# Kernel optimization log

Measured on AMD Instinct MI355X. Metric: run time of the kernel, lower is better.

## Reference

```python
import jax, jax.numpy as jnp
import numpy as np

EPS = 1e-5

def _layernorm(h, g, b):
    mu = jnp.mean(h, axis=-1, keepdims=True)
    var = jnp.mean((h - mu) ** 2, axis=-1, keepdims=True)
    return (h - mu) / jnp.sqrt(var + EPS) * g + b

def _linoss_scan_im(A, dt, Bu):
    # A, dt: (N,) real; Bu: (B, L, N) complex64.
    # IM discretization of z' = -A x + B u, x' = z (LinOSS paper Eq. 3-4),
    # computed with a 2x2 block-diagonal associative (parallel) scan.
    S = 1.0 / (1.0 + dt * dt * A)  # Schur complement
    m11 = 1.0 - dt * dt * A * S
    m12 = -dt * A * S
    m21 = dt * S
    m22 = S
    fz = (m11 * dt) * Bu
    fx = (m21 * dt) * Bu
    Bt, L, N = Bu.shape
    br = lambda m: jnp.broadcast_to(m.astype(Bu.dtype), (Bt, L, N))
    elems = (br(m11), br(m12), br(m21), br(m22), fz, fx)

    def binop(ei, ej):
        a11i, a12i, a21i, a22i, bzi, bxi = ei
        a11j, a12j, a21j, a22j, bzj, bxj = ej
        return (a11j * a11i + a12j * a21i,
                a11j * a12i + a12j * a22i,
                a21j * a11i + a22j * a21i,
                a21j * a12i + a22j * a22i,
                a11j * bzi + a12j * bxi + bzj,
                a21j * bzi + a22j * bxi + bxj)

    res = jax.lax.associative_scan(binop, elems, axis=1)
    return res[5]  # x-component of the state, (B, L, N) complex

def setup_inputs():
    key = jax.random.key(0)
    ks = jax.random.split(key, 20)
    B, L, H_in, D_mod = 8, 2048, 128, 512
    s_in = np.float32(1.0 / np.sqrt(H_in))
    s_d = np.float32(1.0 / np.sqrt(D_mod))
    f32 = jnp.float32
    return {
        "x": jax.random.normal(ks[0], (B, L, H_in), f32),
        "W_in": jax.random.normal(ks[1], (D_mod, H_in), f32) * s_in,
        "b_in": jnp.zeros((D_mod,), f32),
        "W_enc": jax.random.normal(ks[2], (D_mod, D_mod), f32) * s_d,
        "b_enc": jnp.zeros((D_mod,), f32),
        "ln_g": jnp.ones((D_mod,), f32),
        "ln_b": jnp.zeros((D_mod,), f32),
        "A_diag": jax.random.uniform(ks[3], (D_mod,), f32),
        "log_steps": jax.random.normal(ks[4], (D_mod,), f32) * 0.5,
        "B_re": jax.random.normal(ks[5], (D_mod, D_mod), f32) * s_d,
        "B_im": jax.random.normal(ks[6], (D_mod, D_mod), f32) * s_d,
        "C_re": jax.random.normal(ks[7], (D_mod, D_mod), f32) * s_d,
        "C_im": jax.random.normal(ks[8], (D_mod, D_mod), f32) * s_d,
        "D": jax.random.normal(ks[9], (D_mod,), f32),
        "glu_w1": jax.random.normal(ks[10], (D_mod, D_mod), f32) * s_d,
        "glu_b1": jnp.zeros((D_mod,), f32),
        "glu_w2": jax.random.normal(ks[11], (D_mod, D_mod), f32) * s_d,
        "glu_b2": jnp.zeros((D_mod,), f32),
        "W_dec": jax.random.normal(ks[12], (D_mod, D_mod), f32) * s_d,
        "b_dec": jnp.zeros((D_mod,), f32),
        "W_out": jax.random.normal(ks[13], (H_in, D_mod), f32) * s_d,
        "b_out": jnp.zeros((H_in,), f32),
    }

def reference(x, W_in, b_in, W_enc, b_enc, ln_g, ln_b, A_diag, log_steps,
              B_re, B_im, C_re, C_im, D, glu_w1, glu_b1, glu_w2, glu_b2,
              W_dec, b_dec, W_out, b_out):
    h = x @ W_in.T + b_in                       # outer in_proj: (B, L, d)
    h = h @ W_enc.T + b_enc                     # LinOSS encoder
    skip = h
    hn = _layernorm(h, ln_g, ln_b)
    A = jax.nn.relu(A_diag)                     # nonnegative oscillator freqs
    dt = jax.nn.sigmoid(log_steps)              # per-state timestep in (0,1)
    Bc = (B_re + 1j * B_im).astype(jnp.complex64)
    Cc = (C_re + 1j * C_im).astype(jnp.complex64)
    Bu = jnp.einsum('blh,nh->bln', hn.astype(jnp.complex64), Bc)
    xs = _linoss_scan_im(A, dt, Bu)             # (B, L, N) complex
    y = jnp.einsum('bln,hn->blh', xs, Cc).real + D * hn
    y = jax.nn.gelu(y)
    y = (y @ glu_w1.T + glu_b1) * jax.nn.sigmoid(y @ glu_w2.T + glu_b2)  # GLU
    h = skip + y                                # residual (dropout = eval mode)
    h = h @ W_dec.T + b_dec                     # LinOSS decoder
    return h @ W_out.T + b_out                  # outer out_proj: (B, L, out)
```

## Files before the change

### kernel.cpp

```cpp
#include <hip/hip_runtime.h>
#include <cstddef>
#include <cstdint>
#include <math.h>

typedef _Float16 f16;
typedef f16 f16x8 __attribute__((ext_vector_type(8)));
typedef f16 f16x4 __attribute__((ext_vector_type(4)));
typedef float f32x4 __attribute__((ext_vector_type(4)));

constexpr int Bb   = 8;
constexpr int Ll   = 2048;
constexpr int Hin  = 128;
constexpr int Dm   = 512;
constexpr int Mrows = Bb * Ll;
constexpr int NC   = 32;
constexpr int CL   = Ll / NC;
constexpr int SZ1  = Bb * NC * Dm;

constexpr int TILE_ELE = 128 * 64;

static __device__ __forceinline__ float sigmoid_f(float x) {
    return 1.f / (1.f + expf(-x));
}
static __device__ __forceinline__ float gelu_tanh_f(float x) {
    float x3 = x * x * x;
    float t  = tanhf(0.7978845608028654f * (x + 0.044715f * x3));
    return 0.5f * x * (1.f + t);
}

static __device__ __forceinline__ void gld16(const f16* g, f16* l) {
    __builtin_amdgcn_global_load_lds(
        (const __attribute__((address_space(1))) void*)g,
        (__attribute__((address_space(3))) void*)l, 16, 0, 0);
}

__global__ __launch_bounds__(128) void fuse_wc1(
    const float* __restrict__ Wenc, const float* __restrict__ Win,
    const float* __restrict__ b_in, const float* __restrict__ b_enc,
    f16* __restrict__ Wc1, float* __restrict__ bc1)
{
    const int d2 = blockIdx.x;
    const int t  = threadIdx.x;
    float acc = 0.f;
    for (int d = 0; d < Dm; ++d)
        acc = fmaf(Wenc[d2 * Dm + d], Win[d * Hin + t], acc);
    Wc1[d2 * Hin + t] = (f16)acc;
    if (t == 0) {
        float s = 0.f;
        for (int d = 0; d < Dm; ++d) s = fmaf(Wenc[d2 * Dm + d], b_in[d], s);
        bc1[d2] = s + b_enc[d2];
    }
}

__global__ __launch_bounds__(512) void fuse_wc2(
    const float* __restrict__ Wout, const float* __restrict__ Wdec,
    const float* __restrict__ b_dec, const float* __restrict__ b_out,
    f16* __restrict__ Wc2, float* __restrict__ bc2)
{
    const int o = blockIdx.x;
    const int t = threadIdx.x;
    float acc = 0.f;
    for (int d = 0; d < Dm; ++d)
        acc = fmaf(Wout[o * Dm + d], Wdec[d * Dm + t], acc);
    Wc2[o * Dm + t] = (f16)acc;
    if (t == 0) {
        float s = 0.f;
        for (int d = 0; d < Dm; ++d) s = fmaf(Wout[o * Dm + d], b_dec[d], s);
        bc2[o] = s + b_out[o];
    }
}

struct CvtJob { const float* s; f16* d; int n; };
struct CvtJobs { CvtJob j[7]; };

__global__ __launch_bounds__(256) void convert_k(CvtJobs jobs) {
    const CvtJob jb = jobs.j[blockIdx.y];
    const int i = (blockIdx.x * 256 + threadIdx.x) * 4;
    if (i >= jb.n) return;
    const float4 v = *(const float4*)(jb.s + i);
    f16x4 o;
    o.x = (f16)v.x; o.y = (f16)v.y; o.z = (f16)v.z; o.w = (f16)v.w;
    *(f16x4*)(jb.d + i) = o;
}

template <int KM, int OUTF16>
__global__ __launch_bounds__(256) void gemm_mfma(
    const f16* __restrict__ A, const f16* __restrict__ A2,
    const f16* __restrict__ W, const f16* __restrict__ W2,
    const float* __restrict__ bias,
    const f16* __restrict__ EX, const f16* __restrict__ EX2,
    const float* __restrict__ DV,
    void* __restrict__ Cout, int M, int N, int K)
{
    __shared__ f16 smem[4 * TILE_ELE];

    const int tid = threadIdx.x;
    const int l   = tid & 63;
    const int wid = tid >> 6;
    const int wr  = wid >> 1;
    const int wc  = wid & 1;
    const int lc  = l & 15;
    const int lr  = l >> 4;
    const int row0 = blockIdx.x * 128;
    const int col0 = blockIdx.y * 128;

    const int Kst = (KM == 1) ? Dm : K;
    const int KL  = (KM == 1) ? 2 * Dm : K;
    const int NT  = KL >> 6;

    const int swz  = (l & 7) << 4;
    const int off0 = ((lr * 16) ^ swz) >> 1;
    const int off1 = ((64 + lr * 16) ^ swz) >> 1;

    f32x4 acc[4][4];
#pragma unroll
    for (int i = 0; i < 4; ++i)
#pragma unroll
        for (int j = 0; j < 4; ++j) acc[i][j] = (f32x4){0.f, 0.f, 0.f, 0.f};

    auto asrc = [&](int k0) -> const f16* {
        if (KM == 1 && k0 >= Dm) return A2 + (size_t)row0 * Dm + (k0 - Dm);
        return A + (size_t)row0 * Kst + k0;
    };
    auto wsrc = [&](int k0) -> const f16* {
        if (KM == 1 && k0 >= Dm) return W2 + (size_t)col0 * Dm + (k0 - Dm);
        return W + (size_t)col0 * Kst + k0;
    };

#define STAGE(DST, SRC)                                                      \
    {                                                                        \
        _Pragma("unroll")                                                    \
        for (int c = 0; c < 4; ++c) {                                        \
            const int chunk = c * 256 + tid;                                 \
            const int row   = chunk >> 3;                                    \
            const int kb    = ((chunk & 7) << 4) ^ ((row & 7) << 4);         \
            gld16(SRC + (size_t)row * Kst + (kb >> 1), DST + chunk * 8);     \
        }                                                                    \
    }

    STAGE(smem, asrc(0));
    STAGE(smem + 2 * TILE_ELE, wsrc(0));
    __syncthreads();

    int cur = 0;
    for (int kt = 0; kt < NT; ++kt) {
        if (kt + 1 < NT) {
            STAGE(smem + (cur ^ 1) * TILE_ELE, asrc((kt + 1) << 6));
            STAGE(smem + (2 + (cur ^ 1)) * TILE_ELE, wsrc((kt + 1) << 6));
        }
        const f16* Asc = smem + cur * TILE_ELE;
        const f16* Bsc = smem + (2 + cur) * TILE_ELE;
#pragma unroll
        for (int ks = 0; ks < 2; ++ks) {
            const int off = ks ? off1 : off0;
            f16x8 aF[4], bF[4];
#pragma unroll
            for (int mi = 0; mi < 4; ++mi)
                aF[mi] = *(const f16x8*)(Asc + (wr * 64 + mi * 16 + lc) * 64 + off);
#pragma unroll
            for (int ni = 0; ni < 4; ++ni)
                bF[ni] = *(const f16x8*)(Bsc + (wc * 64 + ni * 16 + lc) * 64 + off);
#pragma unroll
            for (int mi = 0; mi < 4; ++mi)
#pragma unroll
                for (int ni = 0; ni < 4; ++ni)
                    acc[mi][ni] = __builtin_amdgcn_mfma_f32_16x16x32_f16(
                        aF[mi], bF[ni], acc[mi][ni], 0, 0, 0);
        }
        __syncthreads();
        cur ^= 1;
    }
#undef STAGE

    float* Cf32 = (float*)Cout;
    f16*   Cf16 = (f16*)Cout;
#pragma unroll
    for (int mi = 0; mi < 4; ++mi) {
#pragma unroll
        for (int ni = 0; ni < 4; ++ni) {
            const int col   = col0 + wc * 64 + ni * 16 + lc;
            const int rbase = row0 + wr * 64 + mi * 16 + lr * 4;
            const f32x4 v = acc[mi][ni];
            if (KM == 0) {
                const float bv = bias ? bias[col] : 0.f;
#pragma unroll
                for (int r = 0; r < 4; ++r) {
                    const float o = v[r] + bv;
                    const size_t idx = (size_t)(rbase + r) * N + col;
                    if (OUTF16) Cf16[idx] = (f16)o; else Cf32[idx] = o;
                }
            } else if (KM == 1) {
                const float dv = DV[col];
#pragma unroll
                for (int r = 0; r < 4; ++r) {
                    const size_t idx = (size_t)(rbase + r) * N + col;
                    const float o = gelu_tanh_f(v[r] + dv * (float)EX[idx]);
                    if (OUTF16) Cf16[idx] = (f16)o; else Cf32[idx] = o;
                }
            } else {
                const float bv = bias[col];
#pragma unroll
                for (int r = 0; r < 4; ++r) {
                    const size_t idx = (size_t)(rbase + r) * N + col;
                    const float o = (float)EX[idx] + (float)EX2[idx] * sigmoid_f(v[r] + bv);
                    if (OUTF16) Cf16[idx] = (f16)o; else Cf32[idx] = o;
                }
            }
        }
    }
}

__global__ __launch_bounds__(256) void layernorm_f16(
    const f16* __restrict__ X, const float* __restrict__ g,
    const float* __restrict__ b, f16* __restrict__ Y)
{
    const int lane = threadIdx.x & 63;
    const int w    = threadIdx.x >> 6;
    const int row  = blockIdx.x * 4 + w;
    const size_t base = (size_t)row * Dm + lane * 8;

    const f16x8 v = *(const f16x8*)(X + base);
    float x[8];
    float s = 0.f, q = 0.f;
#pragma unroll
    for (int i = 0; i < 8; ++i) {
        x[i] = (float)v[i];
        s += x[i]; q += x[i] * x[i];
    }
#pragma unroll
    for (int off = 32; off > 0; off >>= 1) {
        s += __shfl_xor(s, off);
        q += __shfl_xor(q, off);
    }
    const float mu  = s * (1.f / 512.f);
    const float var = q * (1.f / 512.f) - mu * mu;
    const float rs  = rsqrtf(var + 1e-5f);

    const float4 g0 = *(const float4*)(g + lane * 8);
    const float4 g1 = *(const float4*)(g + lane * 8 + 4);
    const float4 b0 = *(const float4*)(b + lane * 8);
    const float4 b1 = *(const float4*)(b + lane * 8 + 4);
    const float gg[8] = {g0.x, g0.y, g0.z, g0.w, g1.x, g1.y, g1.z, g1.w};
    const float bb[8] = {b0.x, b0.y, b0.z, b0.w, b1.x, b1.y, b1.z, b1.w};
    f16x8 o;
#pragma unroll
    for (int i = 0; i < 8; ++i)
        o[i] = (f16)((x[i] - mu) * rs * gg[i] + bb[i]);
    *(f16x8*)(Y + base) = o;
}

__global__ void consts_k(const float* __restrict__ A_diag,
                         const float* __restrict__ log_steps,
                         float* __restrict__ cst)
{
    const int n = threadIdx.x;
    const float a   = fmaxf(A_diag[n], 0.f);
    const float dt  = 1.f / (1.f + expf(-log_steps[n]));
    const float d2a = dt * dt * a;
    const float S   = 1.f / (1.f + d2a);
    const float m11 = 1.f - d2a * S;
    const float m12 = -dt * a * S;
    const float m21 = dt * S;
    const float m22 = S;
    cst[n]            = m11;
    cst[Dm + n]       = m12;
    cst[2 * Dm + n]   = m21;
    cst[3 * Dm + n]   = m22;
    cst[4 * Dm + n]   = m11 * dt;
    cst[5 * Dm + n]   = m21 * dt;
}

__global__ __launch_bounds__(512) void scan_phase1(
    const f16* __restrict__ bur, const f16* __restrict__ bui,
    const float* __restrict__ cst, float* __restrict__ S1)
{
    const int n = threadIdx.x;
    const int c = blockIdx.x & (NC - 1);
    const int b = blockIdx.x >> 5;
    const float m11 = cst[n],          m12 = cst[Dm + n];
    const float m21 = cst[2 * Dm + n], m22 = cst[3 * Dm + n];
    const float c1  = cst[4 * Dm + n], c2  = cst[5 * Dm + n];

    float zr = 0.f, xr = 0.f, zi = 0.f, xi = 0.f;
    const size_t base = ((size_t)b * Ll + (size_t)c * CL) * Dm + n;
#pragma unroll 4
    for (int t = 0; t < CL; ++t) {
        const float br = (float)bur[base + (size_t)t * Dm];
        const float bi = (float)bui[base + (size_t)t * Dm];
        const float zrn = fmaf(m11, zr, fmaf(m12, xr, c1 * br));
        const float xrn = fmaf(m21, zr, fmaf(m22, xr, c2 * br));
        const float zin = fmaf(m11, zi, fmaf(m12, xi, c1 * bi));
        const float xin = fmaf(m21, zi, fmaf(m22, xi, c2 * bi));
        zr = zrn; xr = xrn; zi = zin; xi = xin;
    }
    const int idx = blockIdx.x * Dm + n;
    S1[idx]            = zr;
    S1[SZ1 + idx]      = xr;
    S1[2 * SZ1 + idx]  = zi;
    S1[3 * SZ1 + idx]  = xi;
}

__global__ __launch_bounds__(256) void scan_phase2(
    const float* __restrict__ S1, const float* __restrict__ cst,
    float* __restrict__ G)
{
    const int gidx = blockIdx.x * 256 + threadIdx.x;
    const int n = gidx & (Dm - 1);
    const int b = gidx >> 9;
    const float m11 = cst[n],          m12 = cst[Dm + n];
    const float m21 = cst[2 * Dm + n], m22 = cst[3 * Dm + n];

    float p11 = 1.f, p12 = 0.f, p21 = 0.f, p22 = 1.f;
    for (int i = 0; i < CL; ++i) {
        const float q11 = m11 * p11 + m12 * p21;
        const float q12 = m11 * p12 + m12 * p22;
        const float q21 = m21 * p11 + m22 * p21;
        const float q22 = m21 * p12 + m22 * p22;
        p11 = q11; p12 = q12; p21 = q21; p22 = q22;
    }

    float gzr = 0.f, gxr = 0.f, gzi = 0.f, gxi = 0.f;
    for (int c = 0; c < NC; ++c) {
        const int idx = (b * NC + c) * Dm + n;
        G[idx]           = gzr;
        G[SZ1 + idx]     = gxr;
        G[2 * SZ1 + idx] = gzi;
        G[3 * SZ1 + idx] = gxi;
        const float szr = S1[idx],           sxr = S1[SZ1 + idx];
        const float szi = S1[2 * SZ1 + idx], sxi = S1[3 * SZ1 + idx];
        const float t1 = p11 * gzr + p12 * gxr + szr;
        const float t2 = p21 * gzr + p22 * gxr + sxr;
        const float t3 = p11 * gzi + p12 * gxi + szi;
        const float t4 = p21 * gzi + p22 * gxi + sxi;
        gzr = t1; gxr = t2; gzi = t3; gxi = t4;
    }
}

__global__ __launch_bounds__(512) void scan_phase3(
    const f16* __restrict__ bur, const f16* __restrict__ bui,
    const float* __restrict__ cst, const float* __restrict__ G,
    f16* __restrict__ xrf, f16* __restrict__ xif)
{
    const int n = threadIdx.x;
    const int c = blockIdx.x & (NC - 1);
    const int b = blockIdx.x >> 5;
    const float m11 = cst[n],          m12 = cst[Dm + n];
    const float m21 = cst[2 * Dm + n], m22 = cst[3 * Dm + n];
    const float c1  = cst[4 * Dm + n], c2  = cst[5 * Dm + n];

    const int sidx = blockIdx.x * Dm + n;
    float zr = G[sidx];
    float xr = G[SZ1 + sidx];
    float zi = G[2 * SZ1 + sidx];
    float xi = G[3 * SZ1 + sidx];

    const size_t base = ((size_t)b * Ll + (size_t)c * CL) * Dm + n;
#pragma unroll 4
    for (int t = 0; t < CL; ++t) {
        const float br = (float)bur[base + (size_t)t * Dm];
        const float bi = (float)bui[base + (size_t)t * Dm];
        const float zrn = fmaf(m11, zr, fmaf(m12, xr, c1 * br));
        const float xrn = fmaf(m21, zr, fmaf(m22, xr, c2 * br));
        const float zin = fmaf(m11, zi, fmaf(m12, xi, c1 * bi));
        const float xin = fmaf(m21, zi, fmaf(m22, xi, c2 * bi));
        zr = zrn; xr = xrn; zi = zin; xi = xin;
        xrf[base + (size_t)t * Dm] = (f16)xr;
        xif[base + (size_t)t * Dm] = (f16)(-xi);
    }
}

extern "C" void kernel_launch(void* const* d_in, const int* in_sizes, int n_in,
                              void* d_out, int out_size, void* d_ws, size_t ws_size,
                              hipStream_t stream)
{
    const float* x         = (const float*)d_in[0];
    const float* W_in      = (const float*)d_in[1];
    const float* b_in      = (const float*)d_in[2];
    const float* W_enc     = (const float*)d_in[3];
    const float* b_enc     = (const float*)d_in[4];
    const float* ln_g      = (const float*)d_in[5];
    const float* ln_b      = (const float*)d_in[6];
    const float* A_diag    = (const float*)d_in[7];
    const float* log_steps = (const float*)d_in[8];
    const float* B_re      = (const float*)d_in[9];
    const float* B_im      = (const float*)d_in[10];
    const float* C_re      = (const float*)d_in[11];
    const float* C_im      = (const float*)d_in[12];
    const float* Dv        = (const float*)d_in[13];
    const float* glu_w1    = (const float*)d_in[14];
    const float* glu_b1    = (const float*)d_in[15];
    const float* glu_w2    = (const float*)d_in[16];
    const float* glu_b2    = (const float*)d_in[17];
    const float* W_dec     = (const float*)d_in[18];
    const float* b_dec     = (const float*)d_in[19];
    const float* W_out     = (const float*)d_in[20];
    const float* b_out     = (const float*)d_in[21];

    char* ws = (char*)d_ws;
    const size_t MB = 1 << 20;
    f16*   F2   = (f16*)(ws);
    f16*   F3   = (f16*)(ws + 16 * MB);
    f16*   F0   = (f16*)(ws + 32 * MB);
    f16*   F1   = (f16*)(ws + 48 * MB);
    f16*   BuRh = (f16*)(ws + 64 * MB);
    f16*   BuIh = (f16*)(ws + 80 * MB);
    f16*   P1   = BuRh;
    f16*   GF   = BuIh;
    f16*   XF   = (f16*)(ws + 96 * MB);
    float* S1   = (float*)(ws + 100 * MB);
    float* G    = (float*)(ws + 102 * MB);
    float* cst  = (float*)(ws + 104 * MB);
    f16*   Wc1  = (f16*)(ws + 105 * MB);
    f16*   Wc2  = (f16*)(ws + 106 * MB);
    float* bc1  = (float*)(ws + 107 * MB);
    float* bc2  = (float*)(ws + 107 * MB + 4096);
    f16*   wbuf = (f16*)(ws + 108 * MB);
    f16* BFRE = wbuf;
    f16* BFIM = BFRE + 262144;
    f16* CFRE = BFIM + 262144;
    f16* CFIM = CFRE + 262144;
    f16* W1F  = CFIM + 262144;
    f16* W2F  = W1F  + 262144;

    CvtJobs jobs;
    jobs.j[0] = {x,      XF,   Mrows * Hin};
    jobs.j[1] = {B_re,   BFRE, Dm * Dm};
    jobs.j[2] = {B_im,   BFIM, Dm * Dm};
    jobs.j[3] = {C_re,   CFRE, Dm * Dm};
    jobs.j[4] = {C_im,   CFIM, Dm * Dm};
    jobs.j[5] = {glu_w1, W1F,  Dm * Dm};
    jobs.j[6] = {glu_w2, W2F,  Dm * Dm};

    convert_k<<<dim3((Mrows * Hin) / 1024, 7), 256, 0, stream>>>(jobs);
    fuse_wc1<<<Dm, Hin, 0, stream>>>(W_enc, W_in, b_in, b_enc, Wc1, bc1);
    fuse_wc2<<<Hin, Dm, 0, stream>>>(W_out, W_dec, b_dec, b_out, Wc2, bc2);
    consts_k<<<1, Dm, 0, stream>>>(A_diag, log_steps, cst);

    dim3 blk(256);
    dim3 g512(Mrows / 128, Dm / 128);
    dim3 g128(Mrows / 128, Hin / 128);

    gemm_mfma<0, 1><<<g512, blk, 0, stream>>>(XF, nullptr, Wc1, nullptr, bc1,
                                              nullptr, nullptr, nullptr, F2, Mrows, Dm, Hin);
    layernorm_f16<<<Mrows / 4, 256, 0, stream>>>(F2, ln_g, ln_b, F3);
    gemm_mfma<0, 1><<<g512, blk, 0, stream>>>(F3, nullptr, BFRE, nullptr, nullptr,
                                              nullptr, nullptr, nullptr, BuRh, Mrows, Dm, Dm);
    gemm_mfma<0, 1><<<g512, blk, 0, stream>>>(F3, nullptr, BFIM, nullptr, nullptr,
                                              nullptr, nullptr, nullptr, BuIh, Mrows, Dm, Dm);
    scan_phase1<<<Bb * NC, 512, 0, stream>>>(BuRh, BuIh, cst, S1);
    scan_phase2<<<(Bb * Dm) / 256, 256, 0, stream>>>(S1, cst, G);
    scan_phase3<<<Bb * NC, 512, 0, stream>>>(BuRh, BuIh, cst, G, F0, F1);
    gemm_mfma<1, 1><<<g512, blk, 0, stream>>>(F0, F1, CFRE, CFIM, nullptr,
                                              F3, nullptr, Dv, GF, Mrows, Dm, Dm);
    gemm_mfma<0, 1><<<g512, blk, 0, stream>>>(GF, nullptr, W1F, nullptr, glu_b1,
                                              nullptr, nullptr, nullptr, P1, Mrows, Dm, Dm);
    gemm_mfma<2, 1><<<g512, blk, 0, stream>>>(GF, nullptr, W2F, nullptr, glu_b2,
                                              F2, P1, nullptr, F3, Mrows, Dm, Dm);
    gemm_mfma<0, 0><<<g128, blk, 0, stream>>>(F3, nullptr, Wc2, nullptr, bc2,
                                              nullptr, nullptr, nullptr, (float*)d_out, Mrows, Hin, Dm);
}
```

Before: 332.1 us.

## Concatenate paired GEMMs, fuse GLU gating into final GEMM, drop double buffering

The B_re/B_im projections are merged into one N=1024 GEMM, and likewise the GLU w1/w2 projections. Scan buffers are interleaved with pitch 1024 so the C projection becomes a single K=1024 GEMM. The GLU gating and residual add move into the A-tile load of the final output GEMM, which removes a full intermediate write and read. The GEMM loses its LDS double buffering in favour of single-buffered tiles with higher occupancy hints, which can expose load latency.

```diff
diff --git a/kernel.cpp b/kernel.cpp
--- a/kernel.cpp
+++ b/kernel.cpp
@@ -16,6 +16,7 @@
 constexpr int NC   = 32;
 constexpr int CL   = Ll / NC;
 constexpr int SZ1  = Bb * NC * Dm;
+constexpr int SD   = 1024;
 
 constexpr int TILE_ELE = 128 * 64;
 
@@ -70,7 +71,7 @@
     }
 }
 
-struct CvtJob { const float* s; f16* d; int n; };
+struct CvtJob { const float* s; f16* d; int n; int lgL; int pitch; int off; };
 struct CvtJobs { CvtJob j[7]; };
 
 __global__ __launch_bounds__(256) void convert_k(CvtJobs jobs) {
@@ -78,21 +79,24 @@
     const int i = (blockIdx.x * 256 + threadIdx.x) * 4;
     if (i >= jb.n) return;
     const float4 v = *(const float4*)(jb.s + i);
+    const int row = i >> jb.lgL;
+    const int c   = i & ((1 << jb.lgL) - 1);
     f16x4 o;
     o.x = (f16)v.x; o.y = (f16)v.y; o.z = (f16)v.z; o.w = (f16)v.w;
-    *(f16x4*)(jb.d + i) = o;
+    *(f16x4*)(jb.d + (size_t)row * jb.pitch + jb.off + c) = o;
 }
 
 template <int KM, int OUTF16>
-__global__ __launch_bounds__(256) void gemm_mfma(
-    const f16* __restrict__ A, const f16* __restrict__ A2,
-    const f16* __restrict__ W, const f16* __restrict__ W2,
+__global__ __launch_bounds__(256, (KM == 4) ? 2 : 5) void gemm_mfma(
+    const f16* __restrict__ A, const f16* __restrict__ W,
     const float* __restrict__ bias,
-    const f16* __restrict__ EX, const f16* __restrict__ EX2,
-    const float* __restrict__ DV,
+    const f16* __restrict__ EX, const float* __restrict__ DV,
+    const f16* __restrict__ SK,
     void* __restrict__ Cout, int M, int N, int K)
 {
-    __shared__ f16 smem[4 * TILE_ELE];
+    __shared__ f16 smem[2 * TILE_ELE];
+    f16* As = smem;
+    f16* Bs = smem + TILE_ELE;
 
     const int tid = threadIdx.x;
     const int l   = tid & 63;
@@ -104,10 +108,7 @@
     const int row0 = blockIdx.x * 128;
     const int col0 = blockIdx.y * 128;
 
-    const int Kst = (KM == 1) ? Dm : K;
-    const int KL  = (KM == 1) ? 2 * Dm : K;
-    const int NT  = KL >> 6;
-
+    const int NT = K >> 6;
     const int swz  = (l & 7) << 4;
     const int off0 = ((lr * 16) ^ swz) >> 1;
     const int off1 = ((64 + lr * 16) ^ swz) >> 1;
@@ -118,48 +119,52 @@
 #pragma unroll
         for (int j = 0; j < 4; ++j) acc[i][j] = (f32x4){0.f, 0.f, 0.f, 0.f};
 
-    auto asrc = [&](int k0) -> const f16* {
-        if (KM == 1 && k0 >= Dm) return A2 + (size_t)row0 * Dm + (k0 - Dm);
-        return A + (size_t)row0 * Kst + k0;
-    };
-    auto wsrc = [&](int k0) -> const f16* {
-        if (KM == 1 && k0 >= Dm) return W2 + (size_t)col0 * Dm + (k0 - Dm);
-        return W + (size_t)col0 * Kst + k0;
-    };
-
-#define STAGE(DST, SRC)                                                      \
+#define STAGE(DST, SRC, RS)                                                  \
     {                                                                        \
         _Pragma("unroll")                                                    \
         for (int c = 0; c < 4; ++c) {                                        \
             const int chunk = c * 256 + tid;                                 \
             const int row   = chunk >> 3;                                    \
             const int kb    = ((chunk & 7) << 4) ^ ((row & 7) << 4);         \
-            gld16(SRC + (size_t)row * Kst + (kb >> 1), DST + chunk * 8);     \
+            gld16(SRC + (size_t)row * RS + (kb >> 1), DST + chunk * 8);      \
         }                                                                    \
     }
 
-    STAGE(smem, asrc(0));
-    STAGE(smem + 2 * TILE_ELE, wsrc(0));
-    __syncthreads();
-
-    int cur = 0;
     for (int kt = 0; kt < NT; ++kt) {
-        if (kt + 1 < NT) {
-            STAGE(smem + (cur ^ 1) * TILE_ELE, asrc((kt + 1) << 6));
-            STAGE(smem + (2 + (cur ^ 1)) * TILE_ELE, wsrc((kt + 1) << 6));
+        const int k0 = kt << 6;
+        __syncthreads();
+        if (KM == 4) {
+#pragma unroll
+            for (int c = 0; c < 4; ++c) {
+                const int chunk = c * 256 + tid;
+                const int row   = chunk >> 3;
+                const int ke    = ((((chunk & 7) << 4) ^ ((row & 7) << 4)) >> 1);
+                const size_t pb = (size_t)(row0 + row) * SD + k0 + ke;
+                const f16x8 p1 = *(const f16x8*)(A + pb);
+                const f16x8 p2 = *(const f16x8*)(A + pb + 512);
+                const f16x8 sv = *(const f16x8*)(SK + (size_t)(row0 + row) * 512 + k0 + ke);
+                f16x8 h;
+#pragma unroll
+                for (int j = 0; j < 8; ++j)
+                    h[j] = (f16)((float)sv[j] + (float)p1[j] * sigmoid_f((float)p2[j]));
+                *(f16x8*)(As + chunk * 8) = h;
+            }
+        } else {
+            STAGE(As, A + (size_t)row0 * K + k0, K);
         }
-        const f16* Asc = smem + cur * TILE_ELE;
-        const f16* Bsc = smem + (2 + cur) * TILE_ELE;
+        STAGE(Bs, W + (size_t)col0 * K + k0, K);
+        __syncthreads();
+
 #pragma unroll
         for (int ks = 0; ks < 2; ++ks) {
             const int off = ks ? off1 : off0;
             f16x8 aF[4], bF[4];
 #pragma unroll
             for (int mi = 0; mi < 4; ++mi)
-                aF[mi] = *(const f16x8*)(Asc + (wr * 64 + mi * 16 + lc) * 64 + off);
+                aF[mi] = *(const f16x8*)(As + (wr * 64 + mi * 16 + lc) * 64 + off);
 #pragma unroll
             for (int ni = 0; ni < 4; ++ni)
-                bF[ni] = *(const f16x8*)(Bsc + (wc * 64 + ni * 16 + lc) * 64 + off);
+                bF[ni] = *(const f16x8*)(Bs + (wc * 64 + ni * 16 + lc) * 64 + off);
 #pragma unroll
             for (int mi = 0; mi < 4; ++mi)
 #pragma unroll
@@ -167,8 +172,6 @@
                     acc[mi][ni] = __builtin_amdgcn_mfma_f32_16x16x32_f16(
                         aF[mi], bF[ni], acc[mi][ni], 0, 0, 0);
         }
-        __syncthreads();
-        cur ^= 1;
     }
 #undef STAGE
 
@@ -181,15 +184,7 @@
             const int col   = col0 + wc * 64 + ni * 16 + lc;
             const int rbase = row0 + wr * 64 + mi * 16 + lr * 4;
             const f32x4 v = acc[mi][ni];
-            if (KM == 0) {
-                const float bv = bias ? bias[col] : 0.f;
-#pragma unroll
-                for (int r = 0; r < 4; ++r) {
-                    const float o = v[r] + bv;
-                    const size_t idx = (size_t)(rbase + r) * N + col;
-                    if (OUTF16) Cf16[idx] = (f16)o; else Cf32[idx] = o;
-                }
-            } else if (KM == 1) {
+            if (KM == 1) {
                 const float dv = DV[col];
 #pragma unroll
                 for (int r = 0; r < 4; ++r) {
@@ -198,11 +193,11 @@
                     if (OUTF16) Cf16[idx] = (f16)o; else Cf32[idx] = o;
                 }
             } else {
-                const float bv = bias[col];
+                const float bv = bias ? bias[col] : 0.f;
 #pragma unroll
                 for (int r = 0; r < 4; ++r) {
+                    const float o = v[r] + bv;
                     const size_t idx = (size_t)(rbase + r) * N + col;
-                    const float o = (float)EX[idx] + (float)EX2[idx] * sigmoid_f(v[r] + bv);
                     if (OUTF16) Cf16[idx] = (f16)o; else Cf32[idx] = o;
                 }
             }
@@ -251,7 +246,9 @@
 
 __global__ void consts_k(const float* __restrict__ A_diag,
                          const float* __restrict__ log_steps,
-                         float* __restrict__ cst)
+                         const float* __restrict__ glu_b1,
+                         const float* __restrict__ glu_b2,
+                         float* __restrict__ cst, float* __restrict__ BG)
 {
     const int n = threadIdx.x;
     const float a   = fmaxf(A_diag[n], 0.f);
@@ -268,11 +265,13 @@
     cst[3 * Dm + n]   = m22;
     cst[4 * Dm + n]   = m11 * dt;
     cst[5 * Dm + n]   = m21 * dt;
+    BG[n]       = glu_b1[n];
+    BG[Dm + n]  = glu_b2[n];
 }
 
 __global__ __launch_bounds__(512) void scan_phase1(
-    const f16* __restrict__ bur, const f16* __restrict__ bui,
-    const float* __restrict__ cst, float* __restrict__ S1)
+    const f16* __restrict__ BU, const float* __restrict__ cst,
+    float* __restrict__ S1)
 {
     const int n = threadIdx.x;
     const int c = blockIdx.x & (NC - 1);
@@ -282,11 +281,11 @@
     const float c1  = cst[4 * Dm + n], c2  = cst[5 * Dm + n];
 
     float zr = 0.f, xr = 0.f, zi = 0.f, xi = 0.f;
-    const size_t base = ((size_t)b * Ll + (size_t)c * CL) * Dm + n;
+    const size_t base = ((size_t)b * Ll + (size_t)c * CL) * SD + n;
 #pragma unroll 4
     for (int t = 0; t < CL; ++t) {
-        const float br = (float)bur[base + (size_t)t * Dm];
-        const float bi = (float)bui[base + (size_t)t * Dm];
+        const float br = (float)BU[base + (size_t)t * SD];
+        const float bi = (float)BU[base + (size_t)t * SD + 512];
         const float zrn = fmaf(m11, zr, fmaf(m12, xr, c1 * br));
         const float xrn = fmaf(m21, zr, fmaf(m22, xr, c2 * br));
         const float zin = fmaf(m11, zi, fmaf(m12, xi, c1 * bi));
@@ -337,9 +336,8 @@
 }
 
 __global__ __launch_bounds__(512) void scan_phase3(
-    const f16* __restrict__ bur, const f16* __restrict__ bui,
-    const float* __restrict__ cst, const float* __restrict__ G,
-    f16* __restrict__ xrf, f16* __restrict__ xif)
+    const f16* __restrict__ BU, const float* __restrict__ cst,
+    const float* __restrict__ G, f16* __restrict__ XS)
 {
     const int n = threadIdx.x;
     const int c = blockIdx.x & (NC - 1);
@@ -354,18 +352,18 @@
     float zi = G[2 * SZ1 + sidx];
     float xi = G[3 * SZ1 + sidx];
 
-    const size_t base = ((size_t)b * Ll + (size_t)c * CL) * Dm + n;
+    const size_t base = ((size_t)b * Ll + (size_t)c * CL) * SD + n;
 #pragma unroll 4
     for (int t = 0; t < CL; ++t) {
-        const float br = (float)bur[base + (size_t)t * Dm];
-        const float bi = (float)bui[base + (size_t)t * Dm];
+        const float br = (float)BU[base + (size_t)t * SD];
+        const float bi = (float)BU[base + (size_t)t * SD + 512];
         const float zrn = fmaf(m11, zr, fmaf(m12, xr, c1 * br));
         const float xrn = fmaf(m21, zr, fmaf(m22, xr, c2 * br));
         const float zin = fmaf(m11, zi, fmaf(m12, xi, c1 * bi));
         const float xin = fmaf(m21, zi, fmaf(m22, xi, c2 * bi));
         zr = zrn; xr = xrn; zi = zin; xi = xin;
-        xrf[base + (size_t)t * Dm] = (f16)xr;
-        xif[base + (size_t)t * Dm] = (f16)(-xi);
+        XS[base + (size_t)t * SD]       = (f16)xr;
+        XS[base + (size_t)t * SD + 512] = (f16)(-xi);
     }
 }
 
@@ -398,64 +396,53 @@
 
     char* ws = (char*)d_ws;
     const size_t MB = 1 << 20;
-    f16*   F2   = (f16*)(ws);
-    f16*   F3   = (f16*)(ws + 16 * MB);
-    f16*   F0   = (f16*)(ws + 32 * MB);
-    f16*   F1   = (f16*)(ws + 48 * MB);
-    f16*   BuRh = (f16*)(ws + 64 * MB);
-    f16*   BuIh = (f16*)(ws + 80 * MB);
-    f16*   P1   = BuRh;
-    f16*   GF   = BuIh;
-    f16*   XF   = (f16*)(ws + 96 * MB);
-    float* S1   = (float*)(ws + 100 * MB);
-    float* G    = (float*)(ws + 102 * MB);
-    float* cst  = (float*)(ws + 104 * MB);
-    f16*   Wc1  = (f16*)(ws + 105 * MB);
-    f16*   Wc2  = (f16*)(ws + 106 * MB);
-    float* bc1  = (float*)(ws + 107 * MB);
-    float* bc2  = (float*)(ws + 107 * MB + 4096);
-    f16*   wbuf = (f16*)(ws + 108 * MB);
-    f16* BFRE = wbuf;
-    f16* BFIM = BFRE + 262144;
-    f16* CFRE = BFIM + 262144;
-    f16* CFIM = CFRE + 262144;
-    f16* W1F  = CFIM + 262144;
-    f16* W2F  = W1F  + 262144;
+    f16*   F2  = (f16*)(ws);
+    f16*   F3  = (f16*)(ws + 16 * MB);
+    f16*   XS  = (f16*)(ws + 32 * MB);
+    f16*   BU  = (f16*)(ws + 64 * MB);
+    f16*   Pp  = BU;
+    f16*   GF  = (f16*)(ws + 96 * MB);
+    f16*   XF  = (f16*)(ws + 112 * MB);
+    float* S1  = (float*)(ws + 116 * MB);
+    float* G   = (float*)(ws + 118 * MB);
+    float* cst = (float*)(ws + 120 * MB);
+    float* BG  = (float*)(ws + 120 * MB + 64 * 1024);
+    float* bc1 = (float*)(ws + 120 * MB + 128 * 1024);
+    float* bc2 = (float*)(ws + 120 * MB + 192 * 1024);
+    f16*   WB  = (f16*)(ws + 121 * MB);
+    f16*   WC  = (f16*)(ws + 122 * MB);
+    f16*   WG  = (f16*)(ws + 123 * MB);
+    f16*   Wc1 = (f16*)(ws + 124 * MB);
+    f16*   Wc2 = (f16*)(ws + 124 * MB + 256 * 1024);
 
     CvtJobs jobs;
-    jobs.j[0] = {x,      XF,   Mrows * Hin};
-    jobs.j[1] = {B_re,   BFRE, Dm * Dm};
-    jobs.j[2] = {B_im,   BFIM, Dm * Dm};
-    jobs.j[3] = {C_re,   CFRE, Dm * Dm};
-    jobs.j[4] = {C_im,   CFIM, Dm * Dm};
-    jobs.j[5] = {glu_w1, W1F,  Dm * Dm};
-    jobs.j[6] = {glu_w2, W2F,  Dm * Dm};
+    jobs.j[0] = {x,      XF,            Mrows * Hin, 7, Hin,  0};
+    jobs.j[1] = {B_re,   WB,            Dm * Dm,     9, Dm,   0};
+    jobs.j[2] = {B_im,   WB + 512 * Dm, Dm * Dm,     9, Dm,   0};
+    jobs.j[3] = {C_re,   WC,            Dm * Dm,     9, 1024, 0};
+    jobs.j[4] = {C_im,   WC,            Dm * Dm,     9, 1024, 512};
+    jobs.j[5] = {glu_w1, WG,            Dm * Dm,     9, Dm,   0};
+    jobs.j[6] = {glu_w2, WG + 512 * Dm, Dm * Dm,     9, Dm,   0};
 
     convert_k<<<dim3((Mrows * Hin) / 1024, 7), 256, 0, stream>>>(jobs);
     fuse_wc1<<<Dm, Hin, 0, stream>>>(W_enc, W_in, b_in, b_enc, Wc1, bc1);
     fuse_wc2<<<Hin, Dm, 0, stream>>>(W_out, W_dec, b_dec, b_out, Wc2, bc2);
-    consts_k<<<1, Dm, 0, stream>>>(A_diag, log_steps, cst);
+    consts_k<<<1, Dm, 0, stream>>>(A_diag, log_steps, glu_b1, glu_b2, cst, BG);
 
     dim3 blk(256);
-    dim3 g512(Mrows / 128, Dm / 128);
-    dim3 g128(Mrows / 128, Hin / 128);
-
-    gemm_mfma<0, 1><<<g512, blk, 0, stream>>>(XF, nullptr, Wc1, nullptr, bc1,
-                                              nullptr, nullptr, nullptr, F2, Mrows, Dm, Hin);
+
+    gemm_mfma<0, 1><<<dim3(128, 4), blk, 0, stream>>>(
+        XF, Wc1, bc1, nullptr, nullptr, nullptr, F2, Mrows, Dm, Hin);
     layernorm_f16<<<Mrows / 4, 256, 0, stream>>>(F2, ln_g, ln_b, F3);
-    gemm_mfma<0, 1><<<g512, blk, 0, stream>>>(F3, nullptr, BFRE, nullptr, nullptr,
-                                              nullptr, nullptr, nullptr, BuRh, Mrows, Dm, Dm);
-    gemm_mfma<0, 1><<<g512, blk, 0, stream>>>(F3, nullptr, BFIM, nullptr, nullptr,
-                                              nullptr, nullptr, nullptr, BuIh, Mrows, Dm, Dm);
-    scan_phase1<<<Bb * NC, 512, 0, stream>>>(BuRh, BuIh, cst, S1);
+    gemm_mfma<0, 1><<<dim3(128, 8), blk, 0, stream>>>(
+        F3, WB, nullptr, nullptr, nullptr, nullptr, BU, Mrows, 1024, Dm);
+    scan_phase1<<<Bb * NC, 512, 0, stream>>>(BU, cst, S1);
     scan_phase2<<<(Bb * Dm) / 256, 256, 0, stream>>>(S1, cst, G);
-    scan_phase3<<<Bb * NC, 512, 0, stream>>>(BuRh, BuIh, cst, G, F0, F1);
-    gemm_mfma<1, 1><<<g512, blk, 0, stream>>>(F0, F1, CFRE, CFIM, nullptr,
-                                              F3, nullptr, Dv, GF, Mrows, Dm, Dm);
-    gemm_mfma<0, 1><<<g512, blk, 0, stream>>>(GF, nullptr, W1F, nullptr, glu_b1,
-                                              nullptr, nullptr, nullptr, P1, Mrows, Dm, Dm);
-    gemm_mfma<2, 1><<<g512, blk, 0, stream>>>(GF, nullptr, W2F, nullptr, glu_b2,
-                                              F2, P1, nullptr, F3, Mrows, Dm, Dm);
-    gemm_mfma<0, 0><<<g128, blk, 0, stream>>>(F3, nullptr, Wc2, nullptr, bc2,
-                                              nullptr, nullptr, nullptr, (float*)d_out, Mrows, Hin, Dm);
-}
+    scan_phase3<<<Bb * NC, 512, 0, stream>>>(BU, cst, G, XS);
+    gemm_mfma<1, 1><<<dim3(128, 4), blk, 0, stream>>>(
+        XS, WC, nullptr, F3, Dv, nullptr, GF, Mrows, Dm, 1024);
+    gemm_mfma<0, 1><<<dim3(128, 8), blk, 0, stream>>>(
+        GF, WG, BG, nullptr, nullptr, nullptr, Pp, Mrows, 1024, Dm);
+    gemm_mfma<4, 0><<<dim3(128, 1), blk, 0, stream>>>(
+        Pp, Wc2, bc2, nullptr, nullptr, F2, (float*)d_out, Mrows, Hin, Dm);
+}
```

After: 400.8 us. +20.7%, slower.
